# Kernel optimization log

Hardware: AMD Instinct MI355X
Metric: run time of the kernel (lower is better)

The kernel has to match this reference:

```python
import jax, jax.numpy as jnp
from jax import lax
import numpy as np

HID = 100  # embedding_dim == hidden_dim == 100 (hardcoded in module)
VOCAB = 128000
NUM_CLASSES = 20
SEQ_LEN = 8192


def setup_inputs() -> dict:
    key = jax.random.key(0)
    ks = jax.random.split(key, 8)
    s = 1.0 / np.sqrt(HID)
    return {
        "sequence": jax.random.randint(ks[0], (SEQ_LEN,), 0, VOCAB, dtype=jnp.int64 if jax.config.jax_enable_x64 else jnp.int32),
        "embedding": jax.random.normal(ks[1], (VOCAB, HID), dtype=jnp.float32),
        "W_ih": jax.random.uniform(ks[2], (4 * HID, HID), minval=-s, maxval=s, dtype=jnp.float32),
        "W_hh": jax.random.uniform(ks[3], (4 * HID, HID), minval=-s, maxval=s, dtype=jnp.float32),
        "b_ih": jax.random.uniform(ks[4], (4 * HID,), minval=-s, maxval=s, dtype=jnp.float32),
        "b_hh": jax.random.uniform(ks[5], (4 * HID,), minval=-s, maxval=s, dtype=jnp.float32),
        "fc_w": jax.random.uniform(ks[6], (NUM_CLASSES, HID), minval=-s, maxval=s, dtype=jnp.float32),
        "fc_b": jax.random.uniform(ks[7], (NUM_CLASSES,), minval=-s, maxval=s, dtype=jnp.float32),
    }


def reference(sequence, embedding, W_ih, W_hh, b_ih, b_hh, fc_w, fc_b):
    # embeds: [N, HID] gather from embedding table
    embeds = embedding[sequence]
    # precompute input projections for all timesteps in one GEMM: [N, 4H]
    x_proj = embeds @ W_ih.T + b_ih + b_hh

    def step(carry, xp):
        h, c = carry  # [HID], [HID]
        gates = xp + W_hh @ h  # [4H]; PyTorch gate order i, f, g, o
        i, f, g, o = jnp.split(gates, 4)
        i = jax.nn.sigmoid(i)
        f = jax.nn.sigmoid(f)
        g = jnp.tanh(g)
        o = jax.nn.sigmoid(o)
        c = f * c + i * g
        h = o * jnp.tanh(c)
        return (h, c), None

    h0 = jnp.zeros((HID,), dtype=embeds.dtype)
    c0 = jnp.zeros((HID,), dtype=embeds.dtype)
    (h_last, _), _ = lax.scan(step, (h0, c0), x_proj)
    out = h_last @ fc_w.T + fc_b  # fc on final-timestep output
    return out[None, :]  # view(1, -1)
```

## Files before the change

### kernel.cpp

```cpp
#include <hip/hip_runtime.h>

#define SEQ  8192
#define HID  100
#define G4   400
#define NCLS 20

typedef float v2f __attribute__((ext_vector_type(2)));
typedef float v4f __attribute__((ext_vector_type(4)));

__device__ __forceinline__ float fast_sigmoid(float x) {
    return 1.0f / (1.0f + __expf(-x));
}
__device__ __forceinline__ float fast_tanh(float x) {
    float e = __expf(2.0f * x);
    return 1.0f - 2.0f / (e + 1.0f);
}

__device__ __forceinline__ void wg_barrier() {
    asm volatile("s_waitcnt lgkmcnt(0)" ::: "memory");
    __builtin_amdgcn_s_barrier();
    asm volatile("" ::: "memory");
}

__global__ __launch_bounds__(512)
void xproj_kernel(const int* __restrict__ seq, const float* __restrict__ emb,
                  const float* __restrict__ Wih, const float* __restrict__ bih,
                  const float* __restrict__ bhh, float* __restrict__ xp)
{
    __shared__ float er[16][HID];
    const int tid = threadIdx.x;
    const int t0  = blockIdx.x * 16;

    if (tid < 400) {
        int r = tid / 25, q = tid - r * 25;
        int s = seq[t0 + r];
        *(float4*)&er[r][4 * q] = *(const float4*)&emb[(size_t)s * HID + 4 * q];
    }
    __syncthreads();

    const int row = (tid < G4) ? tid : (G4 - 1);
    const float4* wr = (const float4*)(Wih + (size_t)row * HID);
    const float bias = bih[row] + bhh[row];

    float acc[16];
    #pragma unroll
    for (int u = 0; u < 16; ++u) acc[u] = bias;

    #pragma unroll
    for (int k = 0; k < 25; ++k) {
        float4 wv = wr[k];
        #pragma unroll
        for (int u = 0; u < 16; ++u) {
            float4 ev = *(const float4*)&er[u][4 * k];
            acc[u] = fmaf(wv.x, ev.x, acc[u]);
            acc[u] = fmaf(wv.y, ev.y, acc[u]);
            acc[u] = fmaf(wv.z, ev.z, acc[u]);
            acc[u] = fmaf(wv.w, ev.w, acc[u]);
        }
    }
    if (tid < G4) {
        const int cj = row / HID, rj = row - cj * HID;
        const int pj = rj * 4 + cj;
        #pragma unroll
        for (int u = 0; u < 16; ++u)
            xp[(size_t)(t0 + u) * G4 + pj] = acc[u];
    }
}

template<int MODE>
__global__ __launch_bounds__(512, 2)
void lstm_scan(const float* xp,
               const float* __restrict__ Whh,
               const float* __restrict__ fcw,
               const float* __restrict__ fcb,
               const int* __restrict__ seq, const float* __restrict__ emb,
               const float* __restrict__ Wih, const float* __restrict__ bih,
               const float* __restrict__ bhh,
               float* __restrict__ out)
{
    __shared__ v4f  h4[2][32];
    __shared__ float er_s[HID];

    const int tid = threadIdx.x;
    const int cls = tid & 3;
    const int grp = tid >> 2;
    const int row = (grp < HID) ? grp : (HID - 1);
    const int grow = cls * HID + row;

    v4f wv[25];
    {
        const v4f* wr = (const v4f*)(Whh + (size_t)grow * HID);
        #pragma unroll
        for (int k = 0; k < 25; ++k) wv[k] = wr[k];
        #pragma unroll
        for (int k = 0; k < 25; ++k) asm volatile("" : "+v"(wv[k]));
    }
    float bias2 = 0.0f;
    if constexpr (MODE == 1) bias2 = bih[grow] + bhh[grow];

    if (tid < 128) ((float*)h4)[tid] = 0.0f;
    float c = 0.0f;

    float xn[8];
    if constexpr (MODE == 0) {
        #pragma unroll
        for (int u = 0; u < 8; ++u)
            xn[u] = (tid < G4) ? xp[u * G4 + tid] : 0.0f;
    }
    wg_barrier();

    #pragma unroll 1
    for (int t8 = 0; t8 < SEQ; t8 += 8) {
        #pragma unroll
        for (int u = 0; u < 8; ++u) {
            const int t = t8 + u;
            float xcur;
            if constexpr (MODE == 0) {
                xcur = xn[u];
                if (t + 8 < SEQ && tid < G4)
                    xn[u] = xp[(size_t)(t + 8) * G4 + tid];
            } else {
                int s_ = seq[t];
                if (tid < 25)
                    *(float4*)&er_s[4 * tid] =
                        *(const float4*)&emb[(size_t)s_ * HID + 4 * tid];
                wg_barrier();
                xcur = bias2;
                const float4* xr = (const float4*)(Wih + (size_t)grow * HID);
                #pragma unroll
                for (int k = 0; k < 25; ++k) {
                    float4 wq = xr[k];
                    float4 ev = *(const float4*)&er_s[4 * k];
                    xcur = fmaf(wq.x, ev.x, xcur);
                    xcur = fmaf(wq.y, ev.y, xcur);
                    xcur = fmaf(wq.z, ev.z, xcur);
                    xcur = fmaf(wq.w, ev.w, xcur);
                }
            }

            const v4f* hb = h4[u & 1];
            v2f s0 = {xcur, 0.0f}, s1 = {0.0f, 0.0f};
            v2f s2 = {0.0f, 0.0f}, s3 = {0.0f, 0.0f};
            #pragma unroll
            for (int k = 0; k < 25; ++k) {
                v4f hv = hb[k];
                if (k & 1) {
                    s2 = __builtin_elementwise_fma(wv[k].lo, hv.lo, s2);
                    s3 = __builtin_elementwise_fma(wv[k].hi, hv.hi, s3);
                } else {
                    s0 = __builtin_elementwise_fma(wv[k].lo, hv.lo, s0);
                    s1 = __builtin_elementwise_fma(wv[k].hi, hv.hi, s1);
                }
            }
            v2f sr = (s0 + s2) + (s1 + s3);
            float acc = sr.x + sr.y;

            float a = (cls == 2) ? fast_tanh(acc) : fast_sigmoid(acc);
            float b = __shfl_xor(a, 1);
            float xv = (cls & 1) ? b : a;
            float yv = (cls & 1) ? a : b;
            float x2 = __shfl_xor(xv, 2);
            float y2 = __shfl_xor(yv, 2);
            const bool hi = cls >= 2;
            float gi = hi ? x2 : xv, gg = hi ? xv : x2;
            float gf = hi ? y2 : yv, go = hi ? yv : y2;

            c = fmaf(gf, c, gi * gg);
            float hn = go * fast_tanh(c);
            if (cls == 0 && grp < HID)
                ((float*)h4[(u & 1) ^ 1])[row] = hn;
            wg_barrier();
        }
    }

    if (tid < NCLS) {
        const float* hf = (const float*)h4[0];
        const float* fr = fcw + (size_t)tid * HID;
        float s = fcb[tid];
        #pragma unroll
        for (int k = 0; k < HID; ++k) s = fmaf(fr[k], hf[k], s);
        out[tid] = s;
    }
}

extern "C" void kernel_launch(void* const* d_in, const int* in_sizes, int n_in,
                              void* d_out, int out_size, void* d_ws, size_t ws_size,
                              hipStream_t stream)
{
    const int*   seq = (const int*)d_in[0];
    const float* emb = (const float*)d_in[1];
    const float* Wih = (const float*)d_in[2];
    const float* Whh = (const float*)d_in[3];
    const float* bih = (const float*)d_in[4];
    const float* bhh = (const float*)d_in[5];
    const float* fcw = (const float*)d_in[6];
    const float* fcb = (const float*)d_in[7];
    float* out = (float*)d_out;
    float* xp  = (float*)d_ws;

    const size_t need = (size_t)SEQ * G4 * sizeof(float);
    if (ws_size >= need) {
        xproj_kernel<<<SEQ / 16, 512, 0, stream>>>(seq, emb, Wih, bih, bhh, xp);
        lstm_scan<0><<<1, 512, 0, stream>>>(xp, Whh, fcw, fcb,
                                            seq, emb, Wih, bih, bhh, out);
    } else {
        lstm_scan<1><<<1, 512, 0, stream>>>(nullptr, Whh, fcw, fcb,
                                            seq, emb, Wih, bih, bhh, out);
    }
}
```

Before: 5.881 ms.

## Split LSTM recurrent dot products across quad lanes by K with DPP reduction

Each hidden unit's four gate rows are now handled by a quad of lanes. The work is split along the K dimension: each lane holds a strided slice of all four gate rows of W_hh and computes four partial sums. The partials are combined with DPP quad all-reduces, so every lane gets all gates without the earlier shuffle-based gate exchange. This cuts per-thread LDS reads of h from 25 to 7 vector loads per step and replaces cross-lane shuffles with cheaper DPP adds, at the cost of eight DPP ops plus redundant activation math in every lane. The x-projection is now read as a float4 per hidden unit, which relies on the gate-interleaved layout xproj_kernel already writes.

```diff
diff --git a/kernel.cpp b/kernel.cpp
--- a/kernel.cpp
+++ b/kernel.cpp
@@ -20,6 +20,15 @@
     asm volatile("s_waitcnt lgkmcnt(0)" ::: "memory");
     __builtin_amdgcn_s_barrier();
     asm volatile("" ::: "memory");
+}
+
+template<int CTRL>
+__device__ __forceinline__ float dpp_add(float x) {
+    int p = __builtin_amdgcn_update_dpp(0, __float_as_int(x), CTRL, 0xF, 0xF, true);
+    return x + __int_as_float(p);
+}
+__device__ __forceinline__ float quad_allreduce(float x) {
+    return dpp_add<0x4E>(dpp_add<0xB1>(x));
 }
 
 __global__ __launch_bounds__(512)
@@ -68,7 +77,8 @@
 }
 
 template<int MODE>
-__global__ __launch_bounds__(512, 2)
+__global__ __launch_bounds__(512)
+__attribute__((amdgpu_waves_per_eu(2, 2)))
 void lstm_scan(const float* xp,
                const float* __restrict__ Whh,
                const float* __restrict__ fcw,
@@ -78,34 +88,48 @@
                const float* __restrict__ bhh,
                float* __restrict__ out)
 {
-    __shared__ v4f  h4[2][32];
-    __shared__ float er_s[HID];
+    __shared__ v4f h4[2][32];
+    __shared__ v4f er4[25];
 
     const int tid = threadIdx.x;
-    const int cls = tid & 3;
-    const int grp = tid >> 2;
-    const int row = (grp < HID) ? grp : (HID - 1);
-    const int grow = cls * HID + row;
-
-    v4f wv[25];
-    {
-        const v4f* wr = (const v4f*)(Whh + (size_t)grow * HID);
-        #pragma unroll
-        for (int k = 0; k < 25; ++k) wv[k] = wr[k];
-        #pragma unroll
-        for (int k = 0; k < 25; ++k) asm volatile("" : "+v"(wv[k]));
-    }
-    float bias2 = 0.0f;
-    if constexpr (MODE == 1) bias2 = bih[grow] + bhh[grow];
+    const int s   = tid & 3;
+    const int rg  = tid >> 2;
+    const int r   = (rg < HID) ? rg : (HID - 1);
+    const bool live = (rg < HID);
+
+    v4f w[4][7];
+    #pragma unroll
+    for (int c = 0; c < 4; ++c) {
+        const float* wr = Whh + (size_t)(c * HID + r) * HID;
+        #pragma unroll
+        for (int j = 0; j < 7; ++j) {
+            const int q = (j < 6) ? (s + 4 * j) : 24;
+            v4f t = *(const v4f*)(wr + 4 * q);
+            if (j == 6 && s != 0) t = (v4f){0.f, 0.f, 0.f, 0.f};
+            w[c][j] = t;
+        }
+    }
+    #pragma unroll
+    for (int c = 0; c < 4; ++c)
+        #pragma unroll
+        for (int j = 0; j < 7; ++j)
+            asm volatile("" : "+v"(w[c][j]));
+
+    v4f bias4 = {0.f, 0.f, 0.f, 0.f};
+    if constexpr (MODE == 1) {
+        #pragma unroll
+        for (int c = 0; c < 4; ++c)
+            ((float*)&bias4)[c] = bih[c * HID + r] + bhh[c * HID + r];
+    }
 
     if (tid < 128) ((float*)h4)[tid] = 0.0f;
-    float c = 0.0f;
-
-    float xn[8];
+    float cst = 0.0f;
+
+    v4f xn[8];
     if constexpr (MODE == 0) {
         #pragma unroll
         for (int u = 0; u < 8; ++u)
-            xn[u] = (tid < G4) ? xp[u * G4 + tid] : 0.0f;
+            xn[u] = *(const v4f*)(xp + (size_t)u * G4 + 4 * r);
     }
     wg_barrier();
 
@@ -114,61 +138,68 @@
         #pragma unroll
         for (int u = 0; u < 8; ++u) {
             const int t = t8 + u;
-            float xcur;
+
+            v4f xpv;
             if constexpr (MODE == 0) {
-                xcur = xn[u];
-                if (t + 8 < SEQ && tid < G4)
-                    xn[u] = xp[(size_t)(t + 8) * G4 + tid];
+                xpv = xn[u];
+                if (t + 8 < SEQ)
+                    xn[u] = *(const v4f*)(xp + (size_t)(t + 8) * G4 + 4 * r);
             } else {
-                int s_ = seq[t];
-                if (tid < 25)
-                    *(float4*)&er_s[4 * tid] =
-                        *(const float4*)&emb[(size_t)s_ * HID + 4 * tid];
+                xpv = bias4;
+                if (tid < 25) {
+                    int sq = seq[t];
+                    er4[tid] = *(const v4f*)(emb + (size_t)sq * HID + 4 * tid);
+                }
                 wg_barrier();
-                xcur = bias2;
-                const float4* xr = (const float4*)(Wih + (size_t)grow * HID);
+            }
+
+            const v4f* hb = h4[t & 1];
+            v2f a0 = {0.f,0.f}, a1 = {0.f,0.f}, a2 = {0.f,0.f}, a3 = {0.f,0.f};
+            #pragma unroll
+            for (int j = 0; j < 7; ++j) {
+                const int q = (j < 6) ? (s + 4 * j) : 24;
+                v4f hv = hb[q];
+                a0 = __builtin_elementwise_fma(w[0][j].lo, hv.lo, a0);
+                a0 = __builtin_elementwise_fma(w[0][j].hi, hv.hi, a0);
+                a1 = __builtin_elementwise_fma(w[1][j].lo, hv.lo, a1);
+                a1 = __builtin_elementwise_fma(w[1][j].hi, hv.hi, a1);
+                a2 = __builtin_elementwise_fma(w[2][j].lo, hv.lo, a2);
+                a2 = __builtin_elementwise_fma(w[2][j].hi, hv.hi, a2);
+                a3 = __builtin_elementwise_fma(w[3][j].lo, hv.lo, a3);
+                a3 = __builtin_elementwise_fma(w[3][j].hi, hv.hi, a3);
+            }
+
+            if constexpr (MODE == 1) {
                 #pragma unroll
-                for (int k = 0; k < 25; ++k) {
-                    float4 wq = xr[k];
-                    float4 ev = *(const float4*)&er_s[4 * k];
-                    xcur = fmaf(wq.x, ev.x, xcur);
-                    xcur = fmaf(wq.y, ev.y, xcur);
-                    xcur = fmaf(wq.z, ev.z, xcur);
-                    xcur = fmaf(wq.w, ev.w, xcur);
+                for (int c = 0; c < 4; ++c) {
+                    const float* xr = Wih + (size_t)(c * HID + r) * HID;
+                    #pragma unroll
+                    for (int j = 0; j < 7; ++j) {
+                        if (j == 6 && s != 0) continue;
+                        const int q = (j < 6) ? (s + 4 * j) : 24;
+                        v4f wq = *(const v4f*)(xr + 4 * q);
+                        v4f ev = er4[q];
+                        v2f* ac = (c == 0) ? &a0 : (c == 1) ? &a1 : (c == 2) ? &a2 : &a3;
+                        *ac = __builtin_elementwise_fma(wq.lo, ev.lo, *ac);
+                        *ac = __builtin_elementwise_fma(wq.hi, ev.hi, *ac);
+                    }
                 }
             }
 
-            const v4f* hb = h4[u & 1];
-            v2f s0 = {xcur, 0.0f}, s1 = {0.0f, 0.0f};
-            v2f s2 = {0.0f, 0.0f}, s3 = {0.0f, 0.0f};
-            #pragma unroll
-            for (int k = 0; k < 25; ++k) {
-                v4f hv = hb[k];
-                if (k & 1) {
-                    s2 = __builtin_elementwise_fma(wv[k].lo, hv.lo, s2);
-                    s3 = __builtin_elementwise_fma(wv[k].hi, hv.hi, s3);
-                } else {
-                    s0 = __builtin_elementwise_fma(wv[k].lo, hv.lo, s0);
-                    s1 = __builtin_elementwise_fma(wv[k].hi, hv.hi, s1);
-                }
-            }
-            v2f sr = (s0 + s2) + (s1 + s3);
-            float acc = sr.x + sr.y;
-
-            float a = (cls == 2) ? fast_tanh(acc) : fast_sigmoid(acc);
-            float b = __shfl_xor(a, 1);
-            float xv = (cls & 1) ? b : a;
-            float yv = (cls & 1) ? a : b;
-            float x2 = __shfl_xor(xv, 2);
-            float y2 = __shfl_xor(yv, 2);
-            const bool hi = cls >= 2;
-            float gi = hi ? x2 : xv, gg = hi ? xv : x2;
-            float gf = hi ? y2 : yv, go = hi ? yv : y2;
-
-            c = fmaf(gf, c, gi * gg);
-            float hn = go * fast_tanh(c);
-            if (cls == 0 && grp < HID)
-                ((float*)h4[(u & 1) ^ 1])[row] = hn;
+            float gi = quad_allreduce(a0.x + a0.y) + xpv.x;
+            float gf = quad_allreduce(a1.x + a1.y) + xpv.y;
+            float gg = quad_allreduce(a2.x + a2.y) + xpv.z;
+            float go = quad_allreduce(a3.x + a3.y) + xpv.w;
+
+            gi = fast_sigmoid(gi);
+            gf = fast_sigmoid(gf);
+            gg = fast_tanh(gg);
+            go = fast_sigmoid(go);
+
+            cst = fmaf(gf, cst, gi * gg);
+            float hn = go * fast_tanh(cst);
+            if (live && s == 0)
+                ((float*)h4[(t & 1) ^ 1])[r] = hn;
             wg_barrier();
         }
     }
@@ -176,10 +207,10 @@
     if (tid < NCLS) {
         const float* hf = (const float*)h4[0];
         const float* fr = fcw + (size_t)tid * HID;
-        float s = fcb[tid];
-        #pragma unroll
-        for (int k = 0; k < HID; ++k) s = fmaf(fr[k], hf[k], s);
-        out[tid] = s;
+        float acc = fcb[tid];
+        #pragma unroll
+        for (int k = 0; k < HID; ++k) acc = fmaf(fr[k], hf[k], acc);
+        out[tid] = acc;
     }
 }
 
```

Result: no change. 5.868 ms (-0.2%).
